# Optimization experiments

Hardware: AMD Instinct MI355X
Metric: run time of the kernel (lower is better)

## Reference

```python
import jax, jax.numpy as jnp
import numpy as np
import math

L = 16
DIV = 1e-3        # self.div
SIGMA = 1.0       # soft temperature
HARD_SIGMA = 1e4  # hard temperature


def setup_inputs() -> dict:
    key = jax.random.key(0)
    kx, = jax.random.split(key, 1)
    x = jax.random.normal(kx, (8, 32, 128, 128), dtype=jnp.float32)
    # default mean init: linspace(-(L//2), L//2, L)
    mean = jnp.asarray(np.linspace(-(L // 2), L // 2, L).astype(np.float32))
    log_std = jnp.zeros((L,), dtype=jnp.float32)          # std_list of ones
    log_pi = jnp.full((L,), math.log(1.0 / L), dtype=jnp.float32)  # uniform pi
    return {"x": x, "mean": mean, "log_std": log_std, "log_pi": log_pi}


def reference(x, mean, log_std, log_pi):
    std = jnp.exp(log_std)                      # [L]
    var = std * std + DIV                       # [L]
    # normalized mixing proportions
    mp = jnp.exp(log_pi - jnp.min(log_pi))
    norm_pi = mp / jnp.sum(mp)                  # [L]

    # squared distance to each mean, scaled: [b,c,h,w,L]
    diff = x[..., None] - mean
    dist = (diff * diff) / (2.0 * var)

    inv_norm = norm_pi / jnp.sqrt(2.0 * math.pi * var)  # [L]

    def weighted_softmax(z):
        z = z - jnp.max(z, axis=-1, keepdims=True)
        e = jnp.exp(z) * inv_norm
        return e / jnp.sum(e, axis=-1, keepdims=True)

    phi_soft = weighted_softmax(-SIGMA * dist)
    phi_hard = weighted_softmax(-HARD_SIGMA * dist)

    symbols_hard = jnp.argmax(phi_hard, axis=-1)[..., None]  # [b,c,h,w,1]

    softout = jnp.sum(phi_soft * mean, axis=-1)              # [b,c,h,w]
    hardout = mean[symbols_hard[..., 0]]                     # one-hot @ mean == gather

    q = softout + jax.lax.stop_gradient(hardout - softout)   # straight-through
    return (q, symbols_hard)
```

## Files before the change

### kernel.cpp

```cpp
#include <hip/hip_runtime.h>
#include <math.h>

#define NL 16
#define DIVC 1e-3f

__global__ __launch_bounds__(256) void gmmq_kernel(
    const float* __restrict__ x,
    const float* __restrict__ mean,
    const float* __restrict__ log_std,
    const float* __restrict__ log_pi,
    float* __restrict__ qout,
    float* __restrict__ sout,
    int n4)
{
    __shared__ float s_m[NL + 2], s_tv[NL + 2], s_w[NL + 2];

    const int t = threadIdx.x;
    if (t < NL) {
        float mn = log_pi[0];
        #pragma unroll
        for (int l = 1; l < NL; ++l) mn = fminf(mn, log_pi[l]);
        float sum = 0.f;
        #pragma unroll
        for (int l = 0; l < NL; ++l) sum += expf(log_pi[l] - mn);
        float norm_pi = expf(log_pi[t] - mn) / sum;

        float sd  = expf(log_std[t]);
        float var = sd * sd + DIVC;
        float tv  = 2.0f * var;
        float w   = norm_pi / sqrtf(6.2831853071795864f * var);

        s_m[t + 1]  = mean[t];
        s_tv[t + 1] = tv;
        s_w[t + 1]  = w;
    }
    if (t == 0) {
        s_m[0]  = 1e30f; s_tv[0]  = 1.0f; s_w[0]  = 0.0f;
        s_m[17] = 1e30f; s_tv[17] = 1.0f; s_w[17] = 0.0f;
    }
    __syncthreads();

    const float m0    = s_m[1];
    const float m15   = s_m[16];
    const float invsp = 15.0f / (m15 - m0);
    const float boff  = -m0 * invsp;

    const float4* __restrict__ x4 = (const float4*)x;
    float4* __restrict__ q4 = (float4*)qout;
    float4* __restrict__ s4 = (float4*)sout;

    const int gid    = blockIdx.x * blockDim.x + threadIdx.x;
    const int stride = gridDim.x * blockDim.x;

    for (int i = gid; i < n4; i += stride) {
        float4 xv = x4[i];
        float xa[4] = {xv.x, xv.y, xv.z, xv.w};
        float qa[4], sa[4];

        #pragma unroll
        for (int e = 0; e < 4; ++e) {
            const float xe = xa[e];

            float tf = fmaf(xe, invsp, boff);
            float kf = fminf(fmaxf(__builtin_rintf(tf), 0.0f), 15.0f);
            int   k  = (int)kf;

            float ma = s_m[k],  mb = s_m[k + 1],  mc = s_m[k + 2];
            float ta = s_tv[k], tb = s_tv[k + 1], tc = s_tv[k + 2];
            float wa = s_w[k],  wb = s_w[k + 1],  wc = s_w[k + 2];

            float da = xe - ma, db = xe - mb, dc = xe - mc;
            float za = -1.0e4f * ((da * da) / ta);
            float zb = -1.0e4f * ((db * db) / tb);
            float zc = -1.0e4f * ((dc * dc) / tc);
            float zm = fmaxf(fmaxf(za, zb), zc);
            float ea = __expf(za - zm) * wa;
            float eb = __expf(zb - zm) * wb;
            float ec = __expf(zc - zm) * wc;

            float ebst = ea, mbst = ma; int jb = 0;
            if (eb > ebst) { ebst = eb; mbst = mb; jb = 1; }
            if (ec > ebst) { ebst = ec; mbst = mc; jb = 2; }

            qa[e] = mbst;
            sa[e] = (float)(k - 1 + jb);
        }

        q4[i] = make_float4(qa[0], qa[1], qa[2], qa[3]);
        s4[i] = make_float4(sa[0], sa[1], sa[2], sa[3]);
    }
}

extern "C" void kernel_launch(void* const* d_in, const int* in_sizes, int n_in,
                              void* d_out, int out_size, void* d_ws, size_t ws_size,
                              hipStream_t stream) {
    const float* x       = (const float*)d_in[0];
    const float* mean    = (const float*)d_in[1];
    const float* log_std = (const float*)d_in[2];
    const float* log_pi  = (const float*)d_in[3];

    const int n = in_sizes[0];
    float* qout = (float*)d_out;
    float* sout = qout + n;

    const int n4 = n >> 2;
    const int threads = 256;
    const int blocks  = 2048;

    hipLaunchKernelGGL(gmmq_kernel, dim3(blocks), dim3(threads), 0, stream,
                       x, mean, log_std, log_pi, qout, sout, n4);
}
```

Before: 17.93 us.

## Pack codebook into float4 LDS, test two neighbors, one element per thread

Interleaves mean, 2*var and weight into a single float4 shared array so each candidate needs one LDS load instead of three. Each element now evaluates only the two codebook entries that bracket it rather than three, which cuts the exp and divide work. The grid-stride loop is replaced by one float4 per thread with a launch sized to the data. The risk is that the two-neighbor choice and the changed rounding and clamp order may pick a different symbol than the three-candidate search near midpoints, and the larger grid repeats the per-block setup in more blocks.

```diff
diff --git a/kernel.cpp b/kernel.cpp
--- a/kernel.cpp
+++ b/kernel.cpp
@@ -13,7 +13,7 @@
     float* __restrict__ sout,
     int n4)
 {
-    __shared__ float s_m[NL + 2], s_tv[NL + 2], s_w[NL + 2];
+    __shared__ float4 s_c[NL + 2];
 
     const int t = threadIdx.x;
     if (t < NL) {
@@ -30,65 +30,54 @@
         float tv  = 2.0f * var;
         float w   = norm_pi / sqrtf(6.2831853071795864f * var);
 
-        s_m[t + 1]  = mean[t];
-        s_tv[t + 1] = tv;
-        s_w[t + 1]  = w;
+        s_c[t + 1] = make_float4(mean[t], tv, w, 0.0f);
     }
     if (t == 0) {
-        s_m[0]  = 1e30f; s_tv[0]  = 1.0f; s_w[0]  = 0.0f;
-        s_m[17] = 1e30f; s_tv[17] = 1.0f; s_w[17] = 0.0f;
+        s_c[0]  = make_float4(1e30f, 1.0f, 0.0f, 0.0f);
+        s_c[17] = make_float4(1e30f, 1.0f, 0.0f, 0.0f);
     }
     __syncthreads();
 
-    const float m0    = s_m[1];
-    const float m15   = s_m[16];
+    const float m0    = s_c[1].x;
+    const float m15   = s_c[16].x;
     const float invsp = 15.0f / (m15 - m0);
     const float boff  = -m0 * invsp;
 
-    const float4* __restrict__ x4 = (const float4*)x;
-    float4* __restrict__ q4 = (float4*)qout;
-    float4* __restrict__ s4 = (float4*)sout;
+    const int gid = blockIdx.x * blockDim.x + threadIdx.x;
+    if (gid >= n4) return;
 
-    const int gid    = blockIdx.x * blockDim.x + threadIdx.x;
-    const int stride = gridDim.x * blockDim.x;
+    const float4 xv = ((const float4*)x)[gid];
 
-    for (int i = gid; i < n4; i += stride) {
-        float4 xv = x4[i];
-        float xa[4] = {xv.x, xv.y, xv.z, xv.w};
-        float qa[4], sa[4];
+    float xa[4] = {xv.x, xv.y, xv.z, xv.w};
+    float qa[4], sa[4];
 
-        #pragma unroll
-        for (int e = 0; e < 4; ++e) {
-            const float xe = xa[e];
+    #pragma unroll
+    for (int e = 0; e < 4; ++e) {
+        const float xe = xa[e];
 
-            float tf = fmaf(xe, invsp, boff);
-            float kf = fminf(fmaxf(__builtin_rintf(tf), 0.0f), 15.0f);
-            int   k  = (int)kf;
+        float tf = fmaf(xe, invsp, boff);
+        float tc = fminf(fmaxf(tf, 0.0f), 15.0f);
+        float kf = __builtin_rintf(tc);
+        int   k  = (int)kf;
+        int ilo  = (tc >= kf) ? (k + 1) : k;
 
-            float ma = s_m[k],  mb = s_m[k + 1],  mc = s_m[k + 2];
-            float ta = s_tv[k], tb = s_tv[k + 1], tc = s_tv[k + 2];
-            float wa = s_w[k],  wb = s_w[k + 1],  wc = s_w[k + 2];
+        float4 ca = s_c[ilo];
+        float4 cb = s_c[ilo + 1];
 
-            float da = xe - ma, db = xe - mb, dc = xe - mc;
-            float za = -1.0e4f * ((da * da) / ta);
-            float zb = -1.0e4f * ((db * db) / tb);
-            float zc = -1.0e4f * ((dc * dc) / tc);
-            float zm = fmaxf(fmaxf(za, zb), zc);
-            float ea = __expf(za - zm) * wa;
-            float eb = __expf(zb - zm) * wb;
-            float ec = __expf(zc - zm) * wc;
+        float da = xe - ca.x, db = xe - cb.x;
+        float za = -1.0e4f * ((da * da) / ca.y);
+        float zb = -1.0e4f * ((db * db) / cb.y);
+        float zm = fmaxf(za, zb);
+        float ea = __expf(za - zm) * ca.z;
+        float eb = __expf(zb - zm) * cb.z;
 
-            float ebst = ea, mbst = ma; int jb = 0;
-            if (eb > ebst) { ebst = eb; mbst = mb; jb = 1; }
-            if (ec > ebst) { ebst = ec; mbst = mc; jb = 2; }
+        bool wv = (eb > ea);
+        qa[e] = wv ? cb.x : ca.x;
+        sa[e] = (float)(ilo - 1 + (wv ? 1 : 0));
+    }
 
-            qa[e] = mbst;
-            sa[e] = (float)(k - 1 + jb);
-        }
-
-        q4[i] = make_float4(qa[0], qa[1], qa[2], qa[3]);
-        s4[i] = make_float4(sa[0], sa[1], sa[2], sa[3]);
-    }
+    ((float4*)qout)[gid] = make_float4(qa[0], qa[1], qa[2], qa[3]);
+    ((float4*)sout)[gid] = make_float4(sa[0], sa[1], sa[2], sa[3]);
 }
 
 extern "C" void kernel_launch(void* const* d_in, const int* in_sizes, int n_in,
@@ -105,7 +94,7 @@
 
     const int n4 = n >> 2;
     const int threads = 256;
-    const int blocks  = 2048;
+    const int blocks  = (n4 + threads - 1) / threads;
 
     hipLaunchKernelGGL(gmmq_kernel, dim3(blocks), dim3(threads), 0, stream,
                        x, mean, log_std, log_pi, qout, sout, n4);
```

Measured after the change: 17.84 us. No clear change (-0.5%).
